# Kernel tuning notes

Measured on AMD Instinct MI355X. Metric: run time of the kernel, lower is better.

The kernel has to match this reference:

```python
import jax, jax.numpy as jnp
import numpy as np

N_NODES = 100000
N_EDGES = 300000
D_NODE_IN = 128
D_EDGE_IN = 4
LATENT = 256
HIDDEN = 256
STEPS = 6
D_OUT = 128
LN_EPS = 1e-5


def _mlp(x, w1, b1, w2, b2):
    # hk.nets.MLP([HIDDEN, out], activation=swish): act on hidden, none on output
    return jax.nn.swish(x @ w1 + b1) @ w2 + b2


def _ln(x, scale, offset):
    m = jnp.mean(x, axis=-1, keepdims=True)
    c = x - m
    v = jnp.mean(c * c, axis=-1, keepdims=True)
    return c * jax.lax.rsqrt(v + LN_EPS) * scale + offset


def setup_inputs():
    key = jax.random.key(0)
    ks = iter(jax.random.split(key, 40))

    def w(shape):
        fan_in = shape[-2]
        return (jax.random.normal(next(ks), shape, jnp.float32) / np.sqrt(fan_in).astype(np.float32))

    inp = {}
    inp['node_features'] = jax.random.normal(next(ks), (N_NODES, D_NODE_IN), jnp.float32)
    inp['edge_features'] = jax.random.normal(next(ks), (N_EDGES, D_EDGE_IN), jnp.float32)
    inp['senders'] = jax.random.randint(next(ks), (N_EDGES,), 0, N_NODES, jnp.int32)
    inp['receivers'] = jax.random.randint(next(ks), (N_EDGES,), 0, N_NODES, jnp.int32)
    # encoder (embed) MLPs + LayerNorm
    inp['enc_node_w1'] = w((D_NODE_IN, HIDDEN)); inp['enc_node_b1'] = jnp.zeros((HIDDEN,), jnp.float32)
    inp['enc_node_w2'] = w((HIDDEN, LATENT)); inp['enc_node_b2'] = jnp.zeros((LATENT,), jnp.float32)
    inp['enc_node_ln_s'] = jnp.ones((LATENT,), jnp.float32); inp['enc_node_ln_o'] = jnp.zeros((LATENT,), jnp.float32)
    inp['enc_edge_w1'] = w((D_EDGE_IN, HIDDEN)); inp['enc_edge_b1'] = jnp.zeros((HIDDEN,), jnp.float32)
    inp['enc_edge_w2'] = w((HIDDEN, LATENT)); inp['enc_edge_b2'] = jnp.zeros((LATENT,), jnp.float32)
    inp['enc_edge_ln_s'] = jnp.ones((LATENT,), jnp.float32); inp['enc_edge_ln_o'] = jnp.zeros((LATENT,), jnp.float32)
    # processor: STEPS unshared InteractionNetwork layers, weights stacked on axis 0
    inp['pe_w1'] = w((STEPS, 3 * LATENT, HIDDEN)); inp['pe_b1'] = jnp.zeros((STEPS, HIDDEN), jnp.float32)
    inp['pe_w2'] = w((STEPS, HIDDEN, LATENT)); inp['pe_b2'] = jnp.zeros((STEPS, LATENT), jnp.float32)
    inp['pe_ln_s'] = jnp.ones((STEPS, LATENT), jnp.float32); inp['pe_ln_o'] = jnp.zeros((STEPS, LATENT), jnp.float32)
    inp['pn_w1'] = w((STEPS, 2 * LATENT, HIDDEN)); inp['pn_b1'] = jnp.zeros((STEPS, HIDDEN), jnp.float32)
    inp['pn_w2'] = w((STEPS, HIDDEN, LATENT)); inp['pn_b2'] = jnp.zeros((STEPS, LATENT), jnp.float32)
    inp['pn_ln_s'] = jnp.ones((STEPS, LATENT), jnp.float32); inp['pn_ln_o'] = jnp.zeros((STEPS, LATENT), jnp.float32)
    # decoder (output) MLP, no LayerNorm
    inp['dec_w1'] = w((LATENT, HIDDEN)); inp['dec_b1'] = jnp.zeros((HIDDEN,), jnp.float32)
    inp['dec_w2'] = w((HIDDEN, D_OUT)); inp['dec_b2'] = jnp.zeros((D_OUT,), jnp.float32)
    return inp


def reference(node_features, edge_features, senders, receivers,
              enc_node_w1, enc_node_b1, enc_node_w2, enc_node_b2, enc_node_ln_s, enc_node_ln_o,
              enc_edge_w1, enc_edge_b1, enc_edge_w2, enc_edge_b2, enc_edge_ln_s, enc_edge_ln_o,
              pe_w1, pe_b1, pe_w2, pe_b2, pe_ln_s, pe_ln_o,
              pn_w1, pn_b1, pn_w2, pn_b2, pn_ln_s, pn_ln_o,
              dec_w1, dec_b1, dec_w2, dec_b2):
    # Embed nodes and edges into latent space (MLP + LayerNorm).
    node = _ln(_mlp(node_features, enc_node_w1, enc_node_b1, enc_node_w2, enc_node_b2), enc_node_ln_s, enc_node_ln_o)
    edge = _ln(_mlp(edge_features, enc_edge_w1, enc_edge_b1, enc_edge_w2, enc_edge_b2), enc_edge_ln_s, enc_edge_ln_o)

    n_nodes = node.shape[0]

    def step(carry, p):
        node, edge = carry
        ew1, eb1, ew2, eb2, els, elo, nw1, nb1, nw2, nb2, nls, nlo = p
        # edge update: MLP(concat[edge, sender_node, receiver_node]) + residual
        msg_in = jnp.concatenate([edge, node[senders], node[receivers]], axis=-1)  # [E, 3*LATENT]
        edge = edge + _ln(_mlp(msg_in, ew1, eb1, ew2, eb2), els, elo)
        # aggregate messages to receiver nodes
        agg = jax.ops.segment_sum(edge, receivers, num_segments=n_nodes)  # [N, LATENT]
        # node update: MLP(concat[node, agg]) + residual
        node = node + _ln(_mlp(jnp.concatenate([node, agg], axis=-1), nw1, nb1, nw2, nb2), nls, nlo)
        return (node, edge), None

    (node, edge), _ = jax.lax.scan(
        step, (node, edge),
        (pe_w1, pe_b1, pe_w2, pe_b2, pe_ln_s, pe_ln_o,
         pn_w1, pn_b1, pn_w2, pn_b2, pn_ln_s, pn_ln_o))

    # decoder: plain MLP (no LayerNorm) on nodes only (node_output_size given).
    return _mlp(node, dec_w1, dec_b1, dec_w2, dec_b2)  # [N, D_OUT]
```

## Files before the change

### kernel.cpp

```cpp
#include <hip/hip_runtime.h>
#include <hip/hip_bf16.h>


#define NN 100000
#define NE 300000

typedef __attribute__((ext_vector_type(8))) short bf16x8;
typedef __attribute__((ext_vector_type(8))) unsigned short u16x8;
typedef __attribute__((ext_vector_type(4))) float f32x4;

static __device__ __forceinline__ unsigned short f2bf(float f) {
  union { float f; unsigned u; } v; v.f = f;
  unsigned r = v.u + 0x7FFFu + ((v.u >> 16) & 1u);
  unsigned short h = (unsigned short)(r >> 16);
  if ((h & 0x7F80u) == 0x7F80u) h = 0;
  return h;
}
static __device__ __forceinline__ float bf2f(unsigned short h) {
  union { unsigned u; float f; } v; v.u = ((unsigned)h) << 16;
  return v.f;
}

struct KArgs {
  const float* Xf;
  unsigned short* nodeB;
  unsigned short* edgeB;
  const unsigned short* aggB;
  const int* snd;
  const int* rcv;
  const unsigned short* W1p;
  const unsigned short* W2p;
  const float* b1;
  const float* b2;
  const float* lns;
  const float* lno;
  float* outF;
  int M;
};

__global__ void pack_w(const float* __restrict__ src,
                       unsigned short* __restrict__ dst,
                       int Ksrc, int Kpad, int N) {
  src += (size_t)blockIdx.y * Ksrc * N;
  dst += (size_t)blockIdx.y * Kpad * N;
  int fi = blockIdx.x;
  int nfr = N >> 4;
  int nb = fi % nfr, kb = fi / nfr;
  int t = threadIdx.x;
  int lane = t >> 3, j = t & 7;
  int k = kb * 32 + ((lane >> 4) * 8) + j;
  int col = nb * 16 + (lane & 15);
  unsigned short v = (k < Ksrc) ? f2bf(src[(size_t)k * N + col]) : (unsigned short)0;
  dst[(size_t)fi * 512 + t] = v;
}

__global__ void zero_ws(uint4* __restrict__ p, int n16) {
  uint4 z = {0u, 0u, 0u, 0u};
  for (int i = blockIdx.x * blockDim.x + threadIdx.x; i < n16;
       i += gridDim.x * blockDim.x)
    p[i] = z;
}

__global__ void hist_k(const int* __restrict__ rcv, int* __restrict__ cnt) {
  int e = blockIdx.x * blockDim.x + threadIdx.x;
  if (e < NE) {
    int r = rcv[e]; r = r < 0 ? 0 : (r > NN - 1 ? NN - 1 : r);
    atomicAdd(&cnt[r], 1);
  }
}

__global__ __launch_bounds__(1024)
void scan_k(const int* __restrict__ cnt, int* __restrict__ off) {
  __shared__ int wsum[16];
  __shared__ int carry_s, tot_s;
  int t = threadIdx.x, lane = t & 63, w = t >> 6;
  if (t == 0) carry_s = 0;
  __syncthreads();
  for (int base = 0; base < NN; base += 1024) {
    int i = base + t;
    int v = (i < NN) ? cnt[i] : 0;
    int incl = v;
    #pragma unroll
    for (int d = 1; d < 64; d <<= 1) {
      int u = __shfl_up(incl, d);
      if (lane >= d) incl += u;
    }
    if (lane == 63) wsum[w] = incl;
    int c0 = carry_s;
    __syncthreads();
    if (t < 16) {
      int s = wsum[t];
      int isc = s;
      #pragma unroll
      for (int d = 1; d < 16; d <<= 1) {
        int u = __shfl_up(isc, d);
        if (t >= d) isc += u;
      }
      wsum[t] = isc - s;
    }
    __syncthreads();
    int excl = c0 + wsum[w] + incl - v;
    if (i < NN) off[i] = excl;
    if (t == 1023) tot_s = wsum[15] + incl;
    __syncthreads();
    if (t == 0) carry_s += tot_s;
    __syncthreads();
  }
  if (t == 0) off[NN] = carry_s;
}

__global__ void fill_k(const int* __restrict__ rcv, const int* __restrict__ off,
                       int* __restrict__ cnt2, int* __restrict__ eidx) {
  int e = blockIdx.x * blockDim.x + threadIdx.x;
  if (e < NE) {
    int r = rcv[e]; r = r < 0 ? 0 : (r > NN - 1 ? NN - 1 : r);
    int p = off[r] + atomicAdd(&cnt2[r], 1);
    if (p >= 0 && p < NE) eidx[p] = e;
  }
}

__global__ __launch_bounds__(256)
void agg_k(const unsigned short* __restrict__ edge, const int* __restrict__ off,
           const int* __restrict__ eidx, unsigned short* __restrict__ agg) {
  int t = threadIdx.x;
  int n0 = blockIdx.x * 8;
  #pragma unroll 1
  for (int u = 0; u < 8; ++u) {
    int n = n0 + u;
    if (n >= NN) return;
    int s = off[n], e = off[n + 1];
    if (s < 0) s = 0;
    if (e > NE) e = NE;
    float acc = 0.f;
    for (int i = s; i < e; ++i) {
      int eid = eidx[i];
      eid = eid < 0 ? 0 : (eid > NE - 1 ? NE - 1 : eid);
      acc += bf2f(edge[(size_t)eid * 256 + t]);
    }
    agg[(size_t)n * 256 + t] = f2bf(acc);
  }
}

template<int PHASE>
__global__ __launch_bounds__(512)
void gnn_kernel(KArgs A) {
  constexpr int K1  = PHASE==0?128 : PHASE==1?64 : PHASE==2?768 : PHASE==3?512 : 256;
  constexpr int NS1 = K1 / 64;
  constexpr int N2  = (PHASE==4) ? 128 : 256;
  constexpr int NF2 = N2 / 128;

  __shared__ __align__(16) char smem[52736];
  auto At  = (unsigned short (*)[64][72])smem;
  auto Ht  = (unsigned short (*)[264])(smem + 18432);
  int*   lidx = (int*)(smem + 52224);
  float* ps    = (float*)smem;
  float* ps2   = (float*)(smem + 2048);
  float* rs_mu = (float*)(smem + 4096);
  float* rs_rs = (float*)(smem + 4352);

  const int tid  = threadIdx.x;
  const int wid  = tid >> 6;
  const int lane = tid & 63;
  const int r0   = blockIdx.x * 64;
  const int M    = A.M;

  if constexpr (PHASE == 2) {
    if (tid < 64) {
      int e = r0 + tid; if (e > M - 1) e = M - 1;
      int v = A.snd[e]; v = v < 0 ? 0 : (v > NN - 1 ? NN - 1 : v);
      lidx[tid] = v;
    } else if (tid < 128) {
      int e = r0 + tid - 64; if (e > M - 1) e = M - 1;
      int v = A.rcv[e]; v = v < 0 ? 0 : (v > NN - 1 ? NN - 1 : v);
      lidx[tid] = v;
    }
  }
  __syncthreads();

  auto stage = [&](int ks, int b) {
    int r = tid >> 3;
    int c = tid & 7;
    int row = r0 + r; if (row > M - 1) row = M - 1;
    u16x8 w;
    if constexpr (PHASE == 0) {
      const float* s = A.Xf + (size_t)row * 128 + ks * 64 + c * 8;
      float4 f0 = *(const float4*)s;
      float4 f1 = *(const float4*)(s + 4);
      w[0]=f2bf(f0.x); w[1]=f2bf(f0.y); w[2]=f2bf(f0.z); w[3]=f2bf(f0.w);
      w[4]=f2bf(f1.x); w[5]=f2bf(f1.y); w[6]=f2bf(f1.z); w[7]=f2bf(f1.w);
    } else if constexpr (PHASE == 1) {
      w = (u16x8){0,0,0,0,0,0,0,0};
      if (c == 0) {
        float4 f = *(const float4*)(A.Xf + (size_t)row * 4);
        w[0]=f2bf(f.x); w[1]=f2bf(f.y); w[2]=f2bf(f.z); w[3]=f2bf(f.w);
      }
    } else if constexpr (PHASE == 2) {
      const unsigned short* src;
      if (ks < 4) {
        src = A.edgeB + (size_t)row * 256 + ks * 64 + c * 8;
      } else {
        int nidx = (ks < 8) ? lidx[r] : lidx[64 + r];
        int koff = (ks < 8) ? (ks - 4) * 64 : (ks - 8) * 64;
        src = A.nodeB + (size_t)nidx * 256 + koff + c * 8;
      }
      w = *(const u16x8*)src;
    } else if constexpr (PHASE == 3) {
      const unsigned short* src = (ks < 4)
        ? A.nodeB + (size_t)row * 256 + ks * 64 + c * 8
        : A.aggB  + (size_t)row * 256 + (ks - 4) * 64 + c * 8;
      w = *(const u16x8*)src;
    } else {
      w = *(const u16x8*)(A.nodeB + (size_t)row * 256 + ks * 64 + c * 8);
    }
    *(u16x8*)&At[b][r][c * 8] = w;
  };

  const int mrow  = lane & 15;
  const int kof   = (lane >> 4) * 8;
  const int rbase = (lane >> 4) * 4;

  f32x4 zero4 = {0.f, 0.f, 0.f, 0.f};
  f32x4 acc1[4][2];
  #pragma unroll
  for (int m = 0; m < 4; ++m) { acc1[m][0] = zero4; acc1[m][1] = zero4; }

  stage(0, 0);
  __syncthreads();
  for (int ks = 0; ks < NS1; ++ks) {
    if (ks + 1 < NS1) stage(ks + 1, (ks + 1) & 1);
    #pragma unroll
    for (int kk = 0; kk < 2; ++kk) {
      bf16x8 a0 = *(const bf16x8*)&At[ks & 1][ 0 + mrow][kk * 32 + kof];
      bf16x8 a1 = *(const bf16x8*)&At[ks & 1][16 + mrow][kk * 32 + kof];
      bf16x8 a2 = *(const bf16x8*)&At[ks & 1][32 + mrow][kk * 32 + kof];
      bf16x8 a3 = *(const bf16x8*)&At[ks & 1][48 + mrow][kk * 32 + kof];
      bf16x8 b0 = *(const bf16x8*)(A.W1p + ((size_t)((2 * ks + kk) * 16 + wid * 2 + 0) * 64 + lane) * 8);
      bf16x8 b1 = *(const bf16x8*)(A.W1p + ((size_t)((2 * ks + kk) * 16 + wid * 2 + 1) * 64 + lane) * 8);
      acc1[0][0] = __builtin_amdgcn_mfma_f32_16x16x32_bf16(a0, b0, acc1[0][0], 0, 0, 0);
      acc1[0][1] = __builtin_amdgcn_mfma_f32_16x16x32_bf16(a0, b1, acc1[0][1], 0, 0, 0);
      acc1[1][0] = __builtin_amdgcn_mfma_f32_16x16x32_bf16(a1, b0, acc1[1][0], 0, 0, 0);
      acc1[1][1] = __builtin_amdgcn_mfma_f32_16x16x32_bf16(a1, b1, acc1[1][1], 0, 0, 0);
      acc1[2][0] = __builtin_amdgcn_mfma_f32_16x16x32_bf16(a2, b0, acc1[2][0], 0, 0, 0);
      acc1[2][1] = __builtin_amdgcn_mfma_f32_16x16x32_bf16(a2, b1, acc1[2][1], 0, 0, 0);
      acc1[3][0] = __builtin_amdgcn_mfma_f32_16x16x32_bf16(a3, b0, acc1[3][0], 0, 0, 0);
      acc1[3][1] = __builtin_amdgcn_mfma_f32_16x16x32_bf16(a3, b1, acc1[3][1], 0, 0, 0);
    }
    __syncthreads();
  }

  #pragma unroll
  for (int nf = 0; nf < 2; ++nf) {
    int c = wid * 32 + nf * 16 + mrow;
    float bb = A.b1[c];
    #pragma unroll
    for (int m = 0; m < 4; ++m)
      #pragma unroll
      for (int j = 0; j < 4; ++j) {
        float x = acc1[m][nf][j] + bb;
        float h = x * (1.f / (1.f + __expf(-x)));
        Ht[m * 16 + rbase + j][c] = f2bf(h);
      }
  }
  __syncthreads();

  f32x4 acc2[4][NF2];
  #pragma unroll
  for (int m = 0; m < 4; ++m)
    #pragma unroll
    for (int nf = 0; nf < NF2; ++nf) acc2[m][nf] = zero4;

  #pragma unroll
  for (int ks = 0; ks < 8; ++ks) {
    bf16x8 a[4], b[NF2];
    #pragma unroll
    for (int m = 0; m < 4; ++m)
      a[m] = *(const bf16x8*)&Ht[m * 16 + mrow][ks * 32 + kof];
    #pragma unroll
    for (int nf = 0; nf < NF2; ++nf)
      b[nf] = *(const bf16x8*)(A.W2p + ((size_t)(ks * (N2 / 16) + wid * NF2 + nf) * 64 + lane) * 8);
    #pragma unroll
    for (int m = 0; m < 4; ++m)
      #pragma unroll
      for (int nf = 0; nf < NF2; ++nf)
        acc2[m][nf] = __builtin_amdgcn_mfma_f32_16x16x32_bf16(a[m], b[nf], acc2[m][nf], 0, 0, 0);
  }

  if constexpr (PHASE == 4) {
    int c = wid * 16 + mrow;
    float bb = A.b2[c];
    #pragma unroll
    for (int m = 0; m < 4; ++m)
      #pragma unroll
      for (int j = 0; j < 4; ++j) {
        int rg = r0 + m * 16 + rbase + j;
        if (rg < M) A.outF[(size_t)rg * 128 + c] = acc2[m][0][j] + bb;
      }
  } else {
    const int cc0 = wid * 32 + mrow;
    const int cc1 = cc0 + 16;
    const float bb0 = A.b2[cc0];
    const float bb1 = A.b2[cc1];
    #pragma unroll
    for (int m = 0; m < 4; ++m)
      #pragma unroll
      for (int j = 0; j < 4; ++j) {
        acc2[m][0][j] += bb0;
        acc2[m][1][j] += bb1;
        float t  = acc2[m][0][j] + acc2[m][1][j];
        float t2 = acc2[m][0][j] * acc2[m][0][j] + acc2[m][1][j] * acc2[m][1][j];
        #pragma unroll
        for (int mk = 1; mk < 16; mk <<= 1) {
          t  += __shfl_xor(t, mk);
          t2 += __shfl_xor(t2, mk);
        }
        if (mrow == 0) {
          int row = m * 16 + rbase + j;
          ps [wid * 64 + row] = t;
          ps2[wid * 64 + row] = t2;
        }
      }
    __syncthreads();
    if (tid < 64) {
      float s = 0.f, q = 0.f;
      #pragma unroll
      for (int w = 0; w < 8; ++w) { s += ps[w * 64 + tid]; q += ps2[w * 64 + tid]; }
      float mu = s * (1.0f / 256.0f);
      float va = fmaxf(q * (1.0f / 256.0f) - mu * mu, 0.f);
      rs_mu[tid] = mu;
      rs_rs[tid] = rsqrtf(va + 1e-5f);
    }
    __syncthreads();
    const float ls0 = A.lns[cc0], lo0 = A.lno[cc0];
    const float ls1 = A.lns[cc1], lo1 = A.lno[cc1];
    #pragma unroll
    for (int m = 0; m < 4; ++m)
      #pragma unroll
      for (int j = 0; j < 4; ++j) {
        int row = m * 16 + rbase + j;
        int rg = r0 + row;
        if (rg >= M) continue;
        float mu = rs_mu[row], rstd = rs_rs[row];
        float y0 = (acc2[m][0][j] - mu) * rstd * ls0 + lo0;
        float y1 = (acc2[m][1][j] - mu) * rstd * ls1 + lo1;
        size_t base = (size_t)rg * 256;
        if constexpr (PHASE == 0) {
          A.nodeB[base + cc0] = f2bf(y0);
          A.nodeB[base + cc1] = f2bf(y1);
        } else if constexpr (PHASE == 1) {
          A.edgeB[base + cc0] = f2bf(y0);
          A.edgeB[base + cc1] = f2bf(y1);
        } else if constexpr (PHASE == 2) {
          A.edgeB[base + cc0] = f2bf(bf2f(A.edgeB[base + cc0]) + y0);
          A.edgeB[base + cc1] = f2bf(bf2f(A.edgeB[base + cc1]) + y1);
        } else {
          A.nodeB[base + cc0] = f2bf(bf2f(A.nodeB[base + cc0]) + y0);
          A.nodeB[base + cc1] = f2bf(bf2f(A.nodeB[base + cc1]) + y1);
        }
      }
  }
}

extern "C" void kernel_launch(void* const* d_in, const int* in_sizes, int n_in,
                              void* d_out, int out_size, void* d_ws, size_t ws_size,
                              hipStream_t stream) {
  (void)in_sizes; (void)n_in; (void)out_size; (void)ws_size;
  const float* x_node = (const float*)d_in[0];
  const float* x_edge = (const float*)d_in[1];
  const int* snd = (const int*)d_in[2];
  const int* rcv = (const int*)d_in[3];
  const float* en_w1 = (const float*)d_in[4];
  const float* en_b1 = (const float*)d_in[5];
  const float* en_w2 = (const float*)d_in[6];
  const float* en_b2 = (const float*)d_in[7];
  const float* en_ls = (const float*)d_in[8];
  const float* en_lo = (const float*)d_in[9];
  const float* ee_w1 = (const float*)d_in[10];
  const float* ee_b1 = (const float*)d_in[11];
  const float* ee_w2 = (const float*)d_in[12];
  const float* ee_b2 = (const float*)d_in[13];
  const float* ee_ls = (const float*)d_in[14];
  const float* ee_lo = (const float*)d_in[15];
  const float* pe_w1 = (const float*)d_in[16];
  const float* pe_b1 = (const float*)d_in[17];
  const float* pe_w2 = (const float*)d_in[18];
  const float* pe_b2 = (const float*)d_in[19];
  const float* pe_ls = (const float*)d_in[20];
  const float* pe_lo = (const float*)d_in[21];
  const float* pn_w1 = (const float*)d_in[22];
  const float* pn_b1 = (const float*)d_in[23];
  const float* pn_w2 = (const float*)d_in[24];
  const float* pn_b2 = (const float*)d_in[25];
  const float* pn_ls = (const float*)d_in[26];
  const float* pn_lo = (const float*)d_in[27];
  const float* dc_w1 = (const float*)d_in[28];
  const float* dc_b1 = (const float*)d_in[29];
  const float* dc_w2 = (const float*)d_in[30];
  const float* dc_b2 = (const float*)d_in[31];

  char* ws = (char*)d_ws;
  unsigned short* edgeB = (unsigned short*)(ws);
  unsigned short* nodeB = (unsigned short*)(ws + 153600000LL);
  unsigned short* aggB  = (unsigned short*)(ws + 204800000LL);

  unsigned short* wpck = (unsigned short*)d_out;
  size_t o = 0;
  auto nxt = [&](size_t n) { unsigned short* p = wpck + o; o += n; return p; };
  unsigned short* p_en_w1 = nxt(128 * 256);
  unsigned short* p_en_w2 = nxt(256 * 256);
  unsigned short* p_ee_w1 = nxt(64 * 256);
  unsigned short* p_ee_w2 = nxt(256 * 256);
  unsigned short* p_pe_w1 = nxt((size_t)6 * 768 * 256);
  unsigned short* p_pe_w2 = nxt((size_t)6 * 256 * 256);
  unsigned short* p_pn_w1 = nxt((size_t)6 * 512 * 256);
  unsigned short* p_pn_w2 = nxt((size_t)6 * 256 * 256);
  unsigned short* p_dc_w1 = nxt(256 * 256);
  unsigned short* p_dc_w2 = nxt(256 * 128);
  const size_t DC_BYTES = (256 * 256 + 256 * 128) * 2;

  char* outc = (char*)d_out;
  int* cnt  = (int*)(outc + 6062080);
  int* cnt2 = (int*)(outc + 6462080);
  int* off  = (int*)(outc + 6862080);
  int* eidx = (int*)(outc + 7262096);

  dim3 B(512);
  pack_w<<<dim3(4 * 16, 1), B, 0, stream>>>(en_w1, p_en_w1, 128, 128, 256);
  pack_w<<<dim3(8 * 16, 1), B, 0, stream>>>(en_w2, p_en_w2, 256, 256, 256);
  pack_w<<<dim3(2 * 16, 1), B, 0, stream>>>(ee_w1, p_ee_w1, 4, 64, 256);
  pack_w<<<dim3(8 * 16, 1), B, 0, stream>>>(ee_w2, p_ee_w2, 256, 256, 256);
  pack_w<<<dim3(24 * 16, 6), B, 0, stream>>>(pe_w1, p_pe_w1, 768, 768, 256);
  pack_w<<<dim3(8 * 16, 6), B, 0, stream>>>(pe_w2, p_pe_w2, 256, 256, 256);
  pack_w<<<dim3(16 * 16, 6), B, 0, stream>>>(pn_w1, p_pn_w1, 512, 512, 256);
  pack_w<<<dim3(8 * 16, 6), B, 0, stream>>>(pn_w2, p_pn_w2, 256, 256, 256);
  pack_w<<<dim3(8 * 16, 1), B, 0, stream>>>(dc_w1, p_dc_w1, 256, 256, 256);
  pack_w<<<dim3(8 * 8, 1), B, 0, stream>>>(dc_w2, p_dc_w2, 256, 256, 128);

  zero_ws<<<dim3(196), dim3(256), 0, stream>>>((uint4*)cnt, 800000 / 16);
  hist_k<<<dim3(1172), dim3(256), 0, stream>>>(rcv, cnt);
  scan_k<<<dim3(1), dim3(1024), 0, stream>>>(cnt, off);
  fill_k<<<dim3(1172), dim3(256), 0, stream>>>(rcv, off, cnt2, eidx);

  dim3 GN(1563), GE(4688);

  {
    KArgs a{}; a.Xf = x_node; a.W1p = p_en_w1; a.W2p = p_en_w2;
    a.b1 = en_b1; a.b2 = en_b2; a.lns = en_ls; a.lno = en_lo;
    a.nodeB = nodeB; a.M = NN;
    gnn_kernel<0><<<GN, B, 0, stream>>>(a);
  }
  {
    KArgs a{}; a.Xf = x_edge; a.W1p = p_ee_w1; a.W2p = p_ee_w2;
    a.b1 = ee_b1; a.b2 = ee_b2; a.lns = ee_ls; a.lno = ee_lo;
    a.edgeB = edgeB; a.M = NE;
    gnn_kernel<1><<<GE, B, 0, stream>>>(a);
  }
  for (int s = 0; s < 6; ++s) {
    {
      KArgs a{}; a.snd = snd; a.rcv = rcv;
      a.nodeB = nodeB; a.edgeB = edgeB;
      a.W1p = p_pe_w1 + (size_t)s * 768 * 256;
      a.W2p = p_pe_w2 + (size_t)s * 256 * 256;
      a.b1 = pe_b1 + s * 256; a.b2 = pe_b2 + s * 256;
      a.lns = pe_ls + s * 256; a.lno = pe_lo + s * 256;
      a.M = NE;
      gnn_kernel<2><<<GE, B, 0, stream>>>(a);
    }
    agg_k<<<dim3(12500), dim3(256), 0, stream>>>(edgeB, off, eidx, aggB);
    {
      KArgs a{}; a.nodeB = nodeB; a.aggB = aggB;
      a.W1p = p_pn_w1 + (size_t)s * 512 * 256;
      a.W2p = p_pn_w2 + (size_t)s * 256 * 256;
      a.b1 = pn_b1 + s * 256; a.b2 = pn_b2 + s * 256;
      a.lns = pn_ls + s * 256; a.lno = pn_lo + s * 256;
      a.M = NN;
      gnn_kernel<3><<<GN, B, 0, stream>>>(a);
    }
  }
  hipMemcpyAsync((void*)aggB, p_dc_w1, DC_BYTES, hipMemcpyDeviceToDevice, stream);
  {
    KArgs a{}; a.nodeB = nodeB;
    a.W1p = (const unsigned short*)aggB;
    a.W2p = (const unsigned short*)aggB + 256 * 256;
    a.b1 = dc_b1; a.b2 = dc_b2;
    a.outF = (float*)d_out; a.M = NN;
    gnn_kernel<4><<<GN, B, 0, stream>>>(a);
  }
}
```

Baseline: 3.211 ms.

## Stage A-tiles via direct global-to-LDS loads with XOR-swizzled layout

Replaces register-staged copies of the A operand tiles with global_load_lds 16-byte direct transfers for the bf16 phases. The padded LDS tile layout is replaced by a dense 128-byte-row layout with an XOR swizzle on 16-byte chunks to avoid bank conflicts. This aims to cut VGPR pressure and load-store instruction overhead in the GEMM staging loop. It relies on per-wave contiguous LDS destinations matching the swizzled source addressing and on existing barriers being sufficient for the async loads.

```diff
diff --git a/kernel.cpp b/kernel.cpp
--- a/kernel.cpp
+++ b/kernel.cpp
@@ -8,6 +8,12 @@
 typedef __attribute__((ext_vector_type(8))) short bf16x8;
 typedef __attribute__((ext_vector_type(8))) unsigned short u16x8;
 typedef __attribute__((ext_vector_type(4))) float f32x4;
+
+typedef const __attribute__((address_space(1))) void cg1_t;
+typedef __attribute__((address_space(3))) void l3_t;
+static __device__ __forceinline__ void gld_lds16(const void* g, void* l) {
+  __builtin_amdgcn_global_load_lds((cg1_t*)g, (l3_t*)l, 16, 0, 0);
+}
 
 static __device__ __forceinline__ unsigned short f2bf(float f) {
   union { float f; unsigned u; } v; v.f = f;
@@ -149,10 +155,9 @@
   constexpr int N2  = (PHASE==4) ? 128 : 256;
   constexpr int NF2 = N2 / 128;
 
-  __shared__ __align__(16) char smem[52736];
-  auto At  = (unsigned short (*)[64][72])smem;
-  auto Ht  = (unsigned short (*)[264])(smem + 18432);
-  int*   lidx = (int*)(smem + 52224);
+  __shared__ __align__(16) char smem[50688];
+  auto Ht  = (unsigned short (*)[264])(smem + 16384);
+  int*   lidx = (int*)(smem + 50176);
   float* ps    = (float*)smem;
   float* ps2   = (float*)(smem + 2048);
   float* rs_mu = (float*)(smem + 4096);
@@ -179,45 +184,46 @@
 
   auto stage = [&](int ks, int b) {
     int r = tid >> 3;
-    int c = tid & 7;
+    int c = (tid & 7) ^ (r & 7);
     int row = r0 + r; if (row > M - 1) row = M - 1;
-    u16x8 w;
     if constexpr (PHASE == 0) {
       const float* s = A.Xf + (size_t)row * 128 + ks * 64 + c * 8;
       float4 f0 = *(const float4*)s;
       float4 f1 = *(const float4*)(s + 4);
+      u16x8 w;
       w[0]=f2bf(f0.x); w[1]=f2bf(f0.y); w[2]=f2bf(f0.z); w[3]=f2bf(f0.w);
       w[4]=f2bf(f1.x); w[5]=f2bf(f1.y); w[6]=f2bf(f1.z); w[7]=f2bf(f1.w);
+      *(u16x8*)(smem + b * 8192 + r * 128 + (tid & 7) * 16) = w;
     } else if constexpr (PHASE == 1) {
-      w = (u16x8){0,0,0,0,0,0,0,0};
+      u16x8 w = (u16x8){0,0,0,0,0,0,0,0};
       if (c == 0) {
         float4 f = *(const float4*)(A.Xf + (size_t)row * 4);
         w[0]=f2bf(f.x); w[1]=f2bf(f.y); w[2]=f2bf(f.z); w[3]=f2bf(f.w);
       }
-    } else if constexpr (PHASE == 2) {
+      *(u16x8*)(smem + b * 8192 + r * 128 + (tid & 7) * 16) = w;
+    } else {
       const unsigned short* src;
-      if (ks < 4) {
-        src = A.edgeB + (size_t)row * 256 + ks * 64 + c * 8;
+      if constexpr (PHASE == 2) {
+        if (ks < 4) {
+          src = A.edgeB + (size_t)row * 256 + ks * 64 + c * 8;
+        } else {
+          int nidx = (ks < 8) ? lidx[r] : lidx[64 + r];
+          int koff = (ks < 8) ? (ks - 4) * 64 : (ks - 8) * 64;
+          src = A.nodeB + (size_t)nidx * 256 + koff + c * 8;
+        }
+      } else if constexpr (PHASE == 3) {
+        src = (ks < 4) ? A.nodeB + (size_t)row * 256 + ks * 64 + c * 8
+                       : A.aggB  + (size_t)row * 256 + (ks - 4) * 64 + c * 8;
       } else {
-        int nidx = (ks < 8) ? lidx[r] : lidx[64 + r];
-        int koff = (ks < 8) ? (ks - 4) * 64 : (ks - 8) * 64;
-        src = A.nodeB + (size_t)nidx * 256 + koff + c * 8;
-      }
-      w = *(const u16x8*)src;
-    } else if constexpr (PHASE == 3) {
-      const unsigned short* src = (ks < 4)
-        ? A.nodeB + (size_t)row * 256 + ks * 64 + c * 8
-        : A.aggB  + (size_t)row * 256 + (ks - 4) * 64 + c * 8;
-      w = *(const u16x8*)src;
-    } else {
-      w = *(const u16x8*)(A.nodeB + (size_t)row * 256 + ks * 64 + c * 8);
-    }
-    *(u16x8*)&At[b][r][c * 8] = w;
+        src = A.nodeB + (size_t)row * 256 + ks * 64 + c * 8;
+      }
+      gld_lds16(src, smem + b * 8192 + wid * 1024);
+    }
   };
 
   const int mrow  = lane & 15;
-  const int kof   = (lane >> 4) * 8;
   const int rbase = (lane >> 4) * 4;
+  const int swz   = mrow & 7;
 
   f32x4 zero4 = {0.f, 0.f, 0.f, 0.f};
   f32x4 acc1[4][2];
@@ -228,12 +234,15 @@
   __syncthreads();
   for (int ks = 0; ks < NS1; ++ks) {
     if (ks + 1 < NS1) stage(ks + 1, (ks + 1) & 1);
+    const char* buf = smem + (ks & 1) * 8192;
     #pragma unroll
     for (int kk = 0; kk < 2; ++kk) {
-      bf16x8 a0 = *(const bf16x8*)&At[ks & 1][ 0 + mrow][kk * 32 + kof];
-      bf16x8 a1 = *(const bf16x8*)&At[ks & 1][16 + mrow][kk * 32 + kof];
-      bf16x8 a2 = *(const bf16x8*)&At[ks & 1][32 + mrow][kk * 32 + kof];
-      bf16x8 a3 = *(const bf16x8*)&At[ks & 1][48 + mrow][kk * 32 + kof];
+      int ch = (kk * 4 + (lane >> 4)) ^ swz;
+      const char* p0 = buf + (mrow) * 128 + ch * 16;
+      bf16x8 a0 = *(const bf16x8*)(p0);
+      bf16x8 a1 = *(const bf16x8*)(p0 + 16 * 128);
+      bf16x8 a2 = *(const bf16x8*)(p0 + 32 * 128);
+      bf16x8 a3 = *(const bf16x8*)(p0 + 48 * 128);
       bf16x8 b0 = *(const bf16x8*)(A.W1p + ((size_t)((2 * ks + kk) * 16 + wid * 2 + 0) * 64 + lane) * 8);
       bf16x8 b1 = *(const bf16x8*)(A.W1p + ((size_t)((2 * ks + kk) * 16 + wid * 2 + 1) * 64 + lane) * 8);
       acc1[0][0] = __builtin_amdgcn_mfma_f32_16x16x32_bf16(a0, b0, acc1[0][0], 0, 0, 0);
@@ -269,6 +278,7 @@
     #pragma unroll
     for (int nf = 0; nf < NF2; ++nf) acc2[m][nf] = zero4;
 
+  const int kof = (lane >> 4) * 8;
   #pragma unroll
   for (int ks = 0; ks < 8; ++ks) {
     bf16x8 a[4], b[NF2];
```

Result: no change. 3.191 ms (-0.6%).
